# Performance work log

Hardware: AMD Instinct MI355X
Metric: run time of the kernel (lower is better)

The kernel has to match this reference:

```python
import jax, jax.numpy as jnp
import numpy as np

B, R, C, OUT, IN = 64, 2048, 32, 32, 16
ROUTING_ITERS = 3


def squash(s, axis=-1):
    s_norm = jnp.linalg.norm(s, axis=axis, keepdims=True)
    scale = s_norm ** 2 / (1.0 + s_norm ** 2)
    return scale * s / (s_norm + 1e-8)


def setup_inputs() -> dict:
    key = jax.random.key(0)
    k1, k2 = jax.random.split(key)
    x = jax.random.normal(k1, (B, R, IN), dtype=jnp.float32)
    W = jax.random.normal(k2, (1, R, C, OUT, IN), dtype=jnp.float32)
    return {"x": x, "W": W}


def reference(x, W):
    # u_hat[b,r,c,o] = sum_i W[r,c,o,i] * x[b,r,i]
    u_hat = jnp.einsum('rcoi,bri->brco', W[0], x)  # [B,R,C,OUT]
    b = jnp.zeros((x.shape[0], R, C), dtype=x.dtype)
    v = None
    for i in range(ROUTING_ITERS):
        c = jax.nn.softmax(b, axis=2)[..., None]       # [B,R,C,1]
        s = jnp.sum(c * u_hat, axis=1)                 # [B,C,OUT]
        v = squash(s)                                  # [B,C,OUT]
        if i < ROUTING_ITERS - 1:
            b = b + jnp.einsum('brco,bco->brc', u_hat, v)
    return v
```

## Files before the change

kernel.cpp:

```cpp
#include <hip/hip_runtime.h>


#define Bn 64
#define Rn 2048
#define Cn 32
#define On 32
#define In 16
#define RCH 16
#define NRC2 (Rn / RCH)
#define NG 2

typedef _Float16 half4v __attribute__((ext_vector_type(4)));
typedef float floatx4 __attribute__((ext_vector_type(4)));

template <int PHASE>
__global__ __launch_bounds__(512, 1)
void upass(const float* __restrict__ x, const float* __restrict__ Wfp,
           _Float16* __restrict__ Wh, const float* __restrict__ vroute,
           _Float16* __restrict__ s_part) {
    const int tid  = threadIdx.x;
    const int w    = tid >> 6;
    const int lane = tid & 63;
    const int q    = lane >> 4;
    const int bl   = lane & 15;

    const int L  = blockIdx.x;
    const int bg = (L >> 3) & 1;
    const int rc = (L & 7) | ((L >> 4) << 3);
    const int b0 = bg * 32;

    __shared__ __attribute__((aligned(16))) _Float16 xs[RCH * 32 * 20];
    __shared__ __attribute__((aligned(16))) float sums[2][2][16][8];

    floatx4 v00[4], v01[4], v10[4], v11[4];
    if constexpr (PHASE > 0) {
        const float* vb0 = vroute + (size_t)(b0 + bl) * 1024 + 4 * q;
        const float* vb1 = vroute + (size_t)(b0 + 16 + bl) * 1024 + 4 * q;
#pragma unroll
        for (int t = 0; t < 4; ++t) {
            const int co = (w * 4 + t) * 32;
            v00[t] = *(const floatx4*)(vb0 + co);
            v01[t] = *(const floatx4*)(vb0 + co + 16);
            v10[t] = *(const floatx4*)(vb1 + co);
            v11[t] = *(const floatx4*)(vb1 + co + 16);
        }
    }

#pragma unroll
    for (int k = 0; k < 4; ++k) {
        const int u  = tid + k * 512;
        const int rr = u >> 7, bb = (u >> 2) & 31, iq = u & 3;
        const float4 xv = *(const float4*)(x + (size_t)(b0 + bb) * (Rn * In) +
                                           (size_t)(rc * RCH + rr) * In + iq * 4);
        union { _Float16 h[4]; uint2 u2; } p;
        p.h[0] = (_Float16)xv.x; p.h[1] = (_Float16)xv.y;
        p.h[2] = (_Float16)xv.z; p.h[3] = (_Float16)xv.w;
        *(uint2*)(xs + (rr * 32 + bb) * 20 + iq * 4) = p.u2;
    }
    __syncthreads();

    floatx4 accS0[8], accS1[8];
#pragma unroll
    for (int m = 0; m < 8; ++m) {
        accS0[m] = (floatx4){0.f, 0.f, 0.f, 0.f};
        accS1[m] = (floatx4){0.f, 0.f, 0.f, 0.f};
    }

    const size_t abase = ((size_t)(rc * RCH) * 1024 + w * 128 + bl) * 16 + 4 * q;

    half4v a[8];
    half4v bf0, bf1;
    if constexpr (PHASE > 0) {
        const _Float16* Wp = Wh + abase;
#pragma unroll
        for (int m = 0; m < 8; ++m) a[m] = *(const half4v*)(Wp + m * 256);
        bf0 = *(const half4v*)(xs + bl * 20 + 4 * q);
        bf1 = *(const half4v*)(xs + (16 + bl) * 20 + 4 * q);
    }

    for (int rr = 0; rr < RCH; ++rr) {
        if constexpr (PHASE == 0) {
            const size_t rb = abase + (size_t)rr * 16384;
            const float* Wf = Wfp + rb;
            half4v af[8];
#pragma unroll
            for (int m = 0; m < 8; ++m) {
                const float4 t4 = *(const float4*)(Wf + m * 256);
                af[m] = (half4v){(_Float16)t4.x, (_Float16)t4.y,
                                 (_Float16)t4.z, (_Float16)t4.w};
            }
            if (bg == 0) {
                _Float16* whp = Wh + rb;
#pragma unroll
                for (int m = 0; m < 8; ++m) *(half4v*)(whp + m * 256) = af[m];
            }
            const half4v b0v = *(const half4v*)(xs + (rr * 32 + bl) * 20 + 4 * q);
            const half4v b1v = *(const half4v*)(xs + (rr * 32 + 16 + bl) * 20 + 4 * q);
#pragma unroll
            for (int m = 0; m < 8; ++m) {
                accS0[m] = __builtin_amdgcn_mfma_f32_16x16x16f16(af[m], b0v, accS0[m], 0, 0, 0);
                accS1[m] = __builtin_amdgcn_mfma_f32_16x16x16f16(af[m], b1v, accS1[m], 0, 0, 0);
            }
        } else {
            const int rn = (rr + 1 < RCH) ? rr + 1 : rr;
            const _Float16* Wn = Wh + abase + (size_t)rn * 16384;

            floatx4 D0[8], D1[8];
#pragma unroll
            for (int m = 0; m < 8; ++m) {
                D0[m] = __builtin_amdgcn_mfma_f32_16x16x16f16(
                            a[m], bf0, (floatx4){0.f, 0.f, 0.f, 0.f}, 0, 0, 0);
                D1[m] = __builtin_amdgcn_mfma_f32_16x16x16f16(
                            a[m], bf1, (floatx4){0.f, 0.f, 0.f, 0.f}, 0, 0, 0);
            }

            const half4v bn0 = *(const half4v*)(xs + (rn * 32 + bl) * 20 + 4 * q);
            const half4v bn1 = *(const half4v*)(xs + (rn * 32 + 16 + bl) * 20 + 4 * q);
#pragma unroll
            for (int m = 0; m < 8; ++m) a[m] = *(const half4v*)(Wn + m * 256);
            bf0 = bn0; bf1 = bn1;

            float e0[4], e1[4], se0 = 0.f, se1 = 0.f;
#pragma unroll
            for (int t = 0; t < 4; ++t) {
                float lp0 = D0[2*t].x * v00[t].x + D0[2*t].y * v00[t].y +
                            D0[2*t].z * v00[t].z + D0[2*t].w * v00[t].w +
                            D0[2*t+1].x * v01[t].x + D0[2*t+1].y * v01[t].y +
                            D0[2*t+1].z * v01[t].z + D0[2*t+1].w * v01[t].w;
                float lp1 = D1[2*t].x * v10[t].x + D1[2*t].y * v10[t].y +
                            D1[2*t].z * v10[t].z + D1[2*t].w * v10[t].w +
                            D1[2*t+1].x * v11[t].x + D1[2*t+1].y * v11[t].y +
                            D1[2*t+1].z * v11[t].z + D1[2*t+1].w * v11[t].w;
                lp0 += __shfl_xor(lp0, 16, 64);
                lp0 += __shfl_xor(lp0, 32, 64);
                lp1 += __shfl_xor(lp1, 16, 64);
                lp1 += __shfl_xor(lp1, 32, 64);
                e0[t] = __expf(lp0); se0 += e0[t];
                e1[t] = __expf(lp1); se1 += e1[t];
            }
            if (lane < 32) sums[rr & 1][q][bl][w] = (q == 0) ? se0 : se1;
            asm volatile("s_waitcnt lgkmcnt(0)" ::: "memory");
            __builtin_amdgcn_s_barrier();
            asm volatile("" ::: "memory");
            const floatx4 sa0 = *(const floatx4*)(&sums[rr & 1][0][bl][0]);
            const floatx4 sa1 = *(const floatx4*)(&sums[rr & 1][0][bl][4]);
            const floatx4 sb0 = *(const floatx4*)(&sums[rr & 1][1][bl][0]);
            const floatx4 sb1 = *(const floatx4*)(&sums[rr & 1][1][bl][4]);
            const float tot0 = sa0.x + sa0.y + sa0.z + sa0.w +
                               sa1.x + sa1.y + sa1.z + sa1.w;
            const float tot1 = sb0.x + sb0.y + sb0.z + sb0.w +
                               sb1.x + sb1.y + sb1.z + sb1.w;
            const float winv0 = __builtin_amdgcn_rcpf(tot0);
            const float winv1 = __builtin_amdgcn_rcpf(tot1);
#pragma unroll
            for (int t = 0; t < 4; ++t) {
                const float wt0 = e0[t] * winv0;
                const float wt1 = e1[t] * winv1;
                accS0[2*t]   += wt0 * D0[2*t];
                accS0[2*t+1] += wt0 * D0[2*t+1];
                accS1[2*t]   += wt1 * D1[2*t];
                accS1[2*t+1] += wt1 * D1[2*t+1];
            }
        }
    }

    const size_t sb = (((size_t)rc * 64 + b0 + bl)) * 1024 + w * 128 + 4 * q;
#pragma unroll
    for (int m = 0; m < 8; ++m) {
        const floatx4 a0 = accS0[m], a1 = accS1[m];
        const half4v h0 = {(_Float16)a0.x, (_Float16)a0.y, (_Float16)a0.z, (_Float16)a0.w};
        const half4v h1 = {(_Float16)a1.x, (_Float16)a1.y, (_Float16)a1.z, (_Float16)a1.w};
        *(half4v*)(s_part + sb + m * 16) = h0;
        *(half4v*)(s_part + sb + (size_t)16 * 1024 + m * 16) = h1;
    }
}

__global__ __launch_bounds__(256)
void reduce_squash(const _Float16* __restrict__ sp, float scale,
                   float* __restrict__ vout, const float* __restrict__ vprev,
                   float* __restrict__ vsum) {
    const int b = blockIdx.x >> 3, oct = blockIdx.x & 7;
    const int t = threadIdx.x;
    const int kg = t >> 5, ci = t & 31;
    const size_t base = (size_t)b * 1024 + (size_t)oct * 128 + (size_t)ci * 4;

    floatx4 acc0 = (floatx4){0.f, 0.f, 0.f, 0.f};
    floatx4 acc1 = (floatx4){0.f, 0.f, 0.f, 0.f};
#pragma unroll
    for (int k = kg * 16; k < kg * 16 + 16; k += 2) {
        const half4v h0 = *(const half4v*)(sp + (size_t)k * 65536 + base);
        const half4v h1 = *(const half4v*)(sp + (size_t)(k + 1) * 65536 + base);
        acc0 += (floatx4){(float)h0.x, (float)h0.y, (float)h0.z, (float)h0.w};
        acc1 += (floatx4){(float)h1.x, (float)h1.y, (float)h1.z, (float)h1.w};
    }
    const floatx4 acc = acc0 + acc1;

    __shared__ __attribute__((aligned(16))) float red[8][128];
    *(floatx4*)(&red[kg][ci * 4]) = acc;
    __syncthreads();

    if (t < 128) {
        float s = 0.f;
#pragma unroll
        for (int g = 0; g < 8; ++g) s += red[g][t];
        s *= scale;
        float n2 = s * s;
        n2 += __shfl_xor(n2, 1, 64);
        n2 += __shfl_xor(n2, 2, 64);
        n2 += __shfl_xor(n2, 4, 64);
        n2 += __shfl_xor(n2, 8, 64);
        n2 += __shfl_xor(n2, 16, 64);
        const float norm = sqrtf(n2);
        const float f = (n2 / (1.f + n2)) / (norm + 1e-8f);
        const float vv = s * f;
        const size_t o = (size_t)b * 1024 + (size_t)oct * 128 + t;
        if (vout) vout[o] = vv;
        if (vsum) vsum[o] = vv + vprev[o];
    }
}

extern "C" void kernel_launch(void* const* d_in, const int* in_sizes, int n_in,
                              void* d_out, int out_size, void* d_ws, size_t ws_size,
                              hipStream_t stream) {
    const float* x = (const float*)d_in[0];
    const float* W = (const float*)d_in[1];
    float* out = (float*)d_out;

    char* ws = (char*)d_ws;
    _Float16* Wh     = (_Float16*)ws;
    _Float16* s_part = (_Float16*)(ws + (size_t)67108864);
    float* v1        = (float*)(ws + (size_t)67108864 + 33554432);
    float* v12       = (float*)(ws + (size_t)67108864 + 33554432 + 262144);

    const int ublocks = NG * NRC2;

    upass<0><<<ublocks, 512, 0, stream>>>(x, W, Wh, nullptr, s_part);
    reduce_squash<<<512, 256, 0, stream>>>(s_part, 1.f / 32.f, v1, nullptr, nullptr);

    upass<1><<<ublocks, 512, 0, stream>>>(x, nullptr, Wh, v1, s_part);
    reduce_squash<<<512, 256, 0, stream>>>(s_part, 1.f, nullptr, v1, v12);

    upass<2><<<ublocks, 512, 0, stream>>>(x, nullptr, Wh, v12, s_part);
    reduce_squash<<<512, 256, 0, stream>>>(s_part, 1.f, out, nullptr, nullptr);
}
```

Before: 286.9 us.

## Process two routing rows per barrier and recompute MFMA products instead of storing

The routing pass now handles pairs of input-capsule rows per iteration, so the block-wide softmax-denominator barrier runs once per two rows, with the shared sums buffer widened to match. The u_hat tiles are no longer kept in registers between the logit and accumulation stages. They are recomputed with MFMAs in the second stage, trading extra matrix-core work for lower register pressure and fewer synchronisations. Next-row weight prefetch is restructured around the pair loop.

Measured after the change: 291.9 us. About the same (+1.7%).

```diff
diff --git a/kernel.cpp b/kernel.cpp
--- a/kernel.cpp
+++ b/kernel.cpp
@@ -30,7 +30,7 @@
     const int b0 = bg * 32;
 
     __shared__ __attribute__((aligned(16))) _Float16 xs[RCH * 32 * 20];
-    __shared__ __attribute__((aligned(16))) float sums[2][2][16][8];
+    __shared__ __attribute__((aligned(16))) float sums[2][2][2][16][8];
 
     floatx4 v00[4], v01[4], v10[4], v11[4];
     if constexpr (PHASE > 0) {
@@ -68,18 +68,8 @@
 
     const size_t abase = ((size_t)(rc * RCH) * 1024 + w * 128 + bl) * 16 + 4 * q;
 
-    half4v a[8];
-    half4v bf0, bf1;
-    if constexpr (PHASE > 0) {
-        const _Float16* Wp = Wh + abase;
-#pragma unroll
-        for (int m = 0; m < 8; ++m) a[m] = *(const half4v*)(Wp + m * 256);
-        bf0 = *(const half4v*)(xs + bl * 20 + 4 * q);
-        bf1 = *(const half4v*)(xs + (16 + bl) * 20 + 4 * q);
-    }
-
-    for (int rr = 0; rr < RCH; ++rr) {
-        if constexpr (PHASE == 0) {
+    if constexpr (PHASE == 0) {
+        for (int rr = 0; rr < RCH; ++rr) {
             const size_t rb = abase + (size_t)rr * 16384;
             const float* Wf = Wfp + rb;
             half4v af[8];
@@ -101,75 +91,114 @@
                 accS0[m] = __builtin_amdgcn_mfma_f32_16x16x16f16(af[m], b0v, accS0[m], 0, 0, 0);
                 accS1[m] = __builtin_amdgcn_mfma_f32_16x16x16f16(af[m], b1v, accS1[m], 0, 0, 0);
             }
-        } else {
-            const int rn = (rr + 1 < RCH) ? rr + 1 : rr;
-            const _Float16* Wn = Wh + abase + (size_t)rn * 16384;
-
-            floatx4 D0[8], D1[8];
-#pragma unroll
-            for (int m = 0; m < 8; ++m) {
-                D0[m] = __builtin_amdgcn_mfma_f32_16x16x16f16(
-                            a[m], bf0, (floatx4){0.f, 0.f, 0.f, 0.f}, 0, 0, 0);
-                D1[m] = __builtin_amdgcn_mfma_f32_16x16x16f16(
-                            a[m], bf1, (floatx4){0.f, 0.f, 0.f, 0.f}, 0, 0, 0);
-            }
-
-            const half4v bn0 = *(const half4v*)(xs + (rn * 32 + bl) * 20 + 4 * q);
-            const half4v bn1 = *(const half4v*)(xs + (rn * 32 + 16 + bl) * 20 + 4 * q);
-#pragma unroll
-            for (int m = 0; m < 8; ++m) a[m] = *(const half4v*)(Wn + m * 256);
-            bf0 = bn0; bf1 = bn1;
-
-            float e0[4], e1[4], se0 = 0.f, se1 = 0.f;
+        }
+    } else {
+        half4v a0[8], a1[8], a0n[8];
+#pragma unroll
+        for (int m = 0; m < 8; ++m) a0[m] = *(const half4v*)(Wh + abase + m * 256);
+
+        for (int rr2 = 0; rr2 < RCH; rr2 += 2) {
+            const int buf = (rr2 >> 1) & 1;
+            const _Float16* W1 = Wh + abase + (size_t)(rr2 + 1) * 16384;
+#pragma unroll
+            for (int m = 0; m < 8; ++m) a1[m] = *(const half4v*)(W1 + m * 256);
+            const half4v bf0a = *(const half4v*)(xs + (rr2 * 32 + bl) * 20 + 4 * q);
+            const half4v bf1a = *(const half4v*)(xs + (rr2 * 32 + 16 + bl) * 20 + 4 * q);
+            const half4v bf0b = *(const half4v*)(xs + ((rr2 + 1) * 32 + bl) * 20 + 4 * q);
+            const half4v bf1b = *(const half4v*)(xs + ((rr2 + 1) * 32 + 16 + bl) * 20 + 4 * q);
+
+            float e0a[4], e1a[4], e0b[4], e1b[4];
+            float se0a = 0.f, se1a = 0.f, se0b = 0.f, se1b = 0.f;
 #pragma unroll
             for (int t = 0; t < 4; ++t) {
-                float lp0 = D0[2*t].x * v00[t].x + D0[2*t].y * v00[t].y +
-                            D0[2*t].z * v00[t].z + D0[2*t].w * v00[t].w +
-                            D0[2*t+1].x * v01[t].x + D0[2*t+1].y * v01[t].y +
-                            D0[2*t+1].z * v01[t].z + D0[2*t+1].w * v01[t].w;
-                float lp1 = D1[2*t].x * v10[t].x + D1[2*t].y * v10[t].y +
-                            D1[2*t].z * v10[t].z + D1[2*t].w * v10[t].w +
-                            D1[2*t+1].x * v11[t].x + D1[2*t+1].y * v11[t].y +
-                            D1[2*t+1].z * v11[t].z + D1[2*t+1].w * v11[t].w;
-                lp0 += __shfl_xor(lp0, 16, 64);
-                lp0 += __shfl_xor(lp0, 32, 64);
-                lp1 += __shfl_xor(lp1, 16, 64);
-                lp1 += __shfl_xor(lp1, 32, 64);
-                e0[t] = __expf(lp0); se0 += e0[t];
-                e1[t] = __expf(lp1); se1 += e1[t];
-            }
-            if (lane < 32) sums[rr & 1][q][bl][w] = (q == 0) ? se0 : se1;
+                const floatx4 z = (floatx4){0.f, 0.f, 0.f, 0.f};
+                floatx4 Dx, Dy;
+                Dx = __builtin_amdgcn_mfma_f32_16x16x16f16(a0[2*t],   bf0a, z, 0, 0, 0);
+                Dy = __builtin_amdgcn_mfma_f32_16x16x16f16(a0[2*t+1], bf0a, z, 0, 0, 0);
+                float lp0 = Dx.x*v00[t].x + Dx.y*v00[t].y + Dx.z*v00[t].z + Dx.w*v00[t].w +
+                            Dy.x*v01[t].x + Dy.y*v01[t].y + Dy.z*v01[t].z + Dy.w*v01[t].w;
+                Dx = __builtin_amdgcn_mfma_f32_16x16x16f16(a0[2*t],   bf1a, z, 0, 0, 0);
+                Dy = __builtin_amdgcn_mfma_f32_16x16x16f16(a0[2*t+1], bf1a, z, 0, 0, 0);
+                float lp1 = Dx.x*v10[t].x + Dx.y*v10[t].y + Dx.z*v10[t].z + Dx.w*v10[t].w +
+                            Dy.x*v11[t].x + Dy.y*v11[t].y + Dy.z*v11[t].z + Dy.w*v11[t].w;
+                Dx = __builtin_amdgcn_mfma_f32_16x16x16f16(a1[2*t],   bf0b, z, 0, 0, 0);
+                Dy = __builtin_amdgcn_mfma_f32_16x16x16f16(a1[2*t+1], bf0b, z, 0, 0, 0);
+                float lp2 = Dx.x*v00[t].x + Dx.y*v00[t].y + Dx.z*v00[t].z + Dx.w*v00[t].w +
+                            Dy.x*v01[t].x + Dy.y*v01[t].y + Dy.z*v01[t].z + Dy.w*v01[t].w;
+                Dx = __builtin_amdgcn_mfma_f32_16x16x16f16(a1[2*t],   bf1b, z, 0, 0, 0);
+                Dy = __builtin_amdgcn_mfma_f32_16x16x16f16(a1[2*t+1], bf1b, z, 0, 0, 0);
+                float lp3 = Dx.x*v10[t].x + Dx.y*v10[t].y + Dx.z*v10[t].z + Dx.w*v10[t].w +
+                            Dy.x*v11[t].x + Dy.y*v11[t].y + Dy.z*v11[t].z + Dy.w*v11[t].w;
+
+                lp0 += __shfl_xor(lp0, 16, 64);  lp0 += __shfl_xor(lp0, 32, 64);
+                lp1 += __shfl_xor(lp1, 16, 64);  lp1 += __shfl_xor(lp1, 32, 64);
+                lp2 += __shfl_xor(lp2, 16, 64);  lp2 += __shfl_xor(lp2, 32, 64);
+                lp3 += __shfl_xor(lp3, 16, 64);  lp3 += __shfl_xor(lp3, 32, 64);
+                e0a[t] = __expf(lp0); se0a += e0a[t];
+                e1a[t] = __expf(lp1); se1a += e1a[t];
+                e0b[t] = __expf(lp2); se0b += e0b[t];
+                e1b[t] = __expf(lp3); se1b += e1b[t];
+            }
+            if (lane < 32) {
+                sums[buf][0][q][bl][w] = q ? se1a : se0a;
+                sums[buf][1][q][bl][w] = q ? se1b : se0b;
+            }
             asm volatile("s_waitcnt lgkmcnt(0)" ::: "memory");
             __builtin_amdgcn_s_barrier();
             asm volatile("" ::: "memory");
-            const floatx4 sa0 = *(const floatx4*)(&sums[rr & 1][0][bl][0]);
-            const floatx4 sa1 = *(const floatx4*)(&sums[rr & 1][0][bl][4]);
-            const floatx4 sb0 = *(const floatx4*)(&sums[rr & 1][1][bl][0]);
-            const floatx4 sb1 = *(const floatx4*)(&sums[rr & 1][1][bl][4]);
-            const float tot0 = sa0.x + sa0.y + sa0.z + sa0.w +
-                               sa1.x + sa1.y + sa1.z + sa1.w;
-            const float tot1 = sb0.x + sb0.y + sb0.z + sb0.w +
-                               sb1.x + sb1.y + sb1.z + sb1.w;
-            const float winv0 = __builtin_amdgcn_rcpf(tot0);
-            const float winv1 = __builtin_amdgcn_rcpf(tot1);
+
+            const int rn = (rr2 + 2 < RCH) ? rr2 + 2 : rr2;
+            const _Float16* Wn = Wh + abase + (size_t)rn * 16384;
+#pragma unroll
+            for (int m = 0; m < 8; ++m) a0n[m] = *(const half4v*)(Wn + m * 256);
+
+            const floatx4 sa0 = *(const floatx4*)(&sums[buf][0][0][bl][0]);
+            const floatx4 sa1 = *(const floatx4*)(&sums[buf][0][0][bl][4]);
+            const floatx4 sb0 = *(const floatx4*)(&sums[buf][0][1][bl][0]);
+            const floatx4 sb1 = *(const floatx4*)(&sums[buf][0][1][bl][4]);
+            const floatx4 sc0 = *(const floatx4*)(&sums[buf][1][0][bl][0]);
+            const floatx4 sc1 = *(const floatx4*)(&sums[buf][1][0][bl][4]);
+            const floatx4 sd0 = *(const floatx4*)(&sums[buf][1][1][bl][0]);
+            const floatx4 sd1 = *(const floatx4*)(&sums[buf][1][1][bl][4]);
+            const float winv0a = __builtin_amdgcn_rcpf(
+                sa0.x+sa0.y+sa0.z+sa0.w + sa1.x+sa1.y+sa1.z+sa1.w);
+            const float winv1a = __builtin_amdgcn_rcpf(
+                sb0.x+sb0.y+sb0.z+sb0.w + sb1.x+sb1.y+sb1.z+sb1.w);
+            const float winv0b = __builtin_amdgcn_rcpf(
+                sc0.x+sc0.y+sc0.z+sc0.w + sc1.x+sc1.y+sc1.z+sc1.w);
+            const float winv1b = __builtin_amdgcn_rcpf(
+                sd0.x+sd0.y+sd0.z+sd0.w + sd1.x+sd1.y+sd1.z+sd1.w);
+
 #pragma unroll
             for (int t = 0; t < 4; ++t) {
-                const float wt0 = e0[t] * winv0;
-                const float wt1 = e1[t] * winv1;
-                accS0[2*t]   += wt0 * D0[2*t];
-                accS0[2*t+1] += wt0 * D0[2*t+1];
-                accS1[2*t]   += wt1 * D1[2*t];
-                accS1[2*t+1] += wt1 * D1[2*t+1];
-            }
+                const floatx4 z = (floatx4){0.f, 0.f, 0.f, 0.f};
+                const float wt0a = e0a[t] * winv0a, wt1a = e1a[t] * winv1a;
+                const float wt0b = e0b[t] * winv0b, wt1b = e1b[t] * winv1b;
+                floatx4 Dx, Dy;
+                Dx = __builtin_amdgcn_mfma_f32_16x16x16f16(a0[2*t],   bf0a, z, 0, 0, 0);
+                Dy = __builtin_amdgcn_mfma_f32_16x16x16f16(a0[2*t+1], bf0a, z, 0, 0, 0);
+                accS0[2*t] += wt0a * Dx;  accS0[2*t+1] += wt0a * Dy;
+                Dx = __builtin_amdgcn_mfma_f32_16x16x16f16(a0[2*t],   bf1a, z, 0, 0, 0);
+                Dy = __builtin_amdgcn_mfma_f32_16x16x16f16(a0[2*t+1], bf1a, z, 0, 0, 0);
+                accS1[2*t] += wt1a * Dx;  accS1[2*t+1] += wt1a * Dy;
+                Dx = __builtin_amdgcn_mfma_f32_16x16x16f16(a1[2*t],   bf0b, z, 0, 0, 0);
+                Dy = __builtin_amdgcn_mfma_f32_16x16x16f16(a1[2*t+1], bf0b, z, 0, 0, 0);
+                accS0[2*t] += wt0b * Dx;  accS0[2*t+1] += wt0b * Dy;
+                Dx = __builtin_amdgcn_mfma_f32_16x16x16f16(a1[2*t],   bf1b, z, 0, 0, 0);
+                Dy = __builtin_amdgcn_mfma_f32_16x16x16f16(a1[2*t+1], bf1b, z, 0, 0, 0);
+                accS1[2*t] += wt1b * Dx;  accS1[2*t+1] += wt1b * Dy;
+            }
+#pragma unroll
+            for (int m = 0; m < 8; ++m) a0[m] = a0n[m];
         }
     }
 
     const size_t sb = (((size_t)rc * 64 + b0 + bl)) * 1024 + w * 128 + 4 * q;
 #pragma unroll
     for (int m = 0; m < 8; ++m) {
-        const floatx4 a0 = accS0[m], a1 = accS1[m];
-        const half4v h0 = {(_Float16)a0.x, (_Float16)a0.y, (_Float16)a0.z, (_Float16)a0.w};
-        const half4v h1 = {(_Float16)a1.x, (_Float16)a1.y, (_Float16)a1.z, (_Float16)a1.w};
+        const floatx4 a0v = accS0[m], a1v = accS1[m];
+        const half4v h0 = {(_Float16)a0v.x, (_Float16)a0v.y, (_Float16)a0v.z, (_Float16)a0v.w};
+        const half4v h1 = {(_Float16)a1v.x, (_Float16)a1v.y, (_Float16)a1v.z, (_Float16)a1v.w};
         *(half4v*)(s_part + sb + m * 16) = h0;
         *(half4v*)(s_part + sb + (size_t)16 * 1024 + m * 16) = h1;
     }
```
